# Kernel optimization log

Hardware: AMD Instinct MI355X
Metric: run time of the kernel (lower is better)

The kernel has to match this reference:

```python
import jax, jax.numpy as jnp
import numpy as np

EMBED_DIM = 768
NUM_HEADS = 12


def setup_inputs() -> dict:
    key = jax.random.key(0)
    k_x, k_w1, k_b1, k_w2, k_b2 = jax.random.split(key, 5)
    B, S, D = 4, 2048, EMBED_DIM
    s1 = 1.0 / np.sqrt(D)
    return {
        "x": jax.random.normal(k_x, (B, S, D), dtype=jnp.float32),
        "W1": jax.random.uniform(k_w1, (D, 3 * D), jnp.float32, -s1, s1),  # proj1 weight (in,out)
        "b1": jax.random.uniform(k_b1, (3 * D,), jnp.float32, -s1, s1),
        "W2": jax.random.uniform(k_w2, (D, D), jnp.float32, -s1, s1),  # proj2 weight (in,out)
        "b2": jax.random.uniform(k_b2, (D,), jnp.float32, -s1, s1),
    }


def reference(x, W1, b1, W2, b2):
    B, S, D = x.shape
    H = NUM_HEADS
    h = D // H
    qkv = x @ W1 + b1                       # [B,S,3D]
    qkv = qkv.reshape(B, S, H, 3 * h).transpose(0, 2, 1, 3)  # [B,H,S,3h]
    # chunk order in the original: K, Q, V
    K = qkv[..., :h]
    Q = qkv[..., h:2 * h]
    V = qkv[..., 2 * h:]
    # NOTE: original code computes Q @ V^T (not Q @ K^T) -- reproduced faithfully
    scores = jnp.einsum("bhqd,bhkd->bhqk", Q, V) / jnp.sqrt(jnp.float32(h))
    att = jax.nn.softmax(scores, axis=-1)
    out = jnp.einsum("bhqk,bhkd->bhqd", att, V)  # [B,H,S,h]
    out = out.transpose(0, 2, 1, 3).reshape(B, S, D)
    return out @ W2 + b2
```

## Files before the change

kernel.cpp:

```cpp
#include <hip/hip_runtime.h>
#include <hip/hip_bf16.h>
#include <math.h>


#define SEQ   2048
#define DIM   768
#define NHEAD 12
#define HDIM  64
#define BATCH 4

#define QSCALE 0.1803368801111244f

typedef __attribute__((ext_vector_type(8))) short s16x8;
typedef __attribute__((ext_vector_type(4))) float f32x4;

#if __has_builtin(__builtin_amdgcn_exp2f)
#define EXP2F(x) __builtin_amdgcn_exp2f(x)
#else
#define EXP2F(x) exp2f(x)
#endif

__device__ __forceinline__ unsigned short f2bf(float f) {
    union { float f; unsigned int u; } v; v.f = f;
    unsigned int r = v.u + 0x7fffu + ((v.u >> 16) & 1u);
    return (unsigned short)(r >> 16);
}

__device__ __forceinline__ unsigned int cvt_pk_bf16(float a, float b) {
    unsigned int r;
    asm("v_cvt_pk_bf16_f32 %0, %1, %2" : "=v"(r) : "v"(a), "v"(b));
    return r;
}

__device__ __forceinline__ void gload_lds16(const void* g, void* l) {
    __builtin_amdgcn_global_load_lds(
        (const __attribute__((address_space(1))) unsigned int*)g,
        (__attribute__((address_space(3))) unsigned int*)l, 16, 0, 0);
}

__global__ __launch_bounds__(256) void cvt_all(
    const float* __restrict__ x, const float* __restrict__ W1,
    const float* __restrict__ W2, unsigned short* __restrict__ xb,
    unsigned short* __restrict__ W1bt, unsigned short* __restrict__ W2bt)
{
    __shared__ float T[32][33];
    const int id = blockIdx.x;

    if (id >= 1728) {
        const size_t i4 = ((size_t)(id - 1728) * 256 + threadIdx.x) * 4;
        float4 v = *(const float4*)&x[i4];
        ushort4 o;
        o.x = f2bf(v.x); o.y = f2bf(v.y); o.z = f2bf(v.z); o.w = f2bf(v.w);
        *(ushort4*)&xb[i4] = o;
        return;
    }

    const float* W;
    unsigned short* out;
    int n0, k0, src_ld, c0;
    if (id < 1152) {
        W = W1; out = W1bt; src_ld = 2304;
        n0 = (id % 48) * 32; k0 = (id / 48) * 32;
        c0 = (n0 >> 7) * 192 + 64 + (n0 & 127);
    } else {
        const int id2 = id - 1152;
        W = W2; out = W2bt; src_ld = DIM;
        n0 = (id2 % 24) * 32; k0 = (id2 / 24) * 32;
        c0 = n0;
    }
    const int tc = threadIdx.x & 31, tr = threadIdx.x >> 5;
    #pragma unroll
    for (int i = 0; i < 4; ++i)
        T[tr + i * 8][tc] = W[(size_t)(k0 + tr + i * 8) * src_ld + c0 + tc];
    __syncthreads();
    #pragma unroll
    for (int i = 0; i < 4; ++i)
        out[(size_t)(n0 + tr + i * 8) * DIM + k0 + tc] = f2bf(T[tc][tr + i * 8]);
}

__device__ __forceinline__ void gemm128_loop(
    const unsigned short* __restrict__ A, const unsigned short* __restrict__ B,
    unsigned short* As, unsigned short* Bs, int m0, int n0, f32x4 acc[4][4])
{
    const int tid  = threadIdx.x;
    const int wave = tid >> 6;
    const int lane = tid & 63;
    const int quad = lane >> 4;
    const int lcol = lane & 15;
    const int wm = wave >> 1, wn = wave & 1;

    const int sr = lane >> 2;
    const int sp = lane & 3;
    const int sc = sp ^ ((sr >> 1) & 3);

    const int aswz = ((quad ^ ((lcol >> 1) & 3)) << 4);

    for (int k0 = 0; k0 < DIM; k0 += 32) {
        #pragma unroll
        for (int s = 0; s < 2; ++s) {
            const int r0 = wave * 32 + s * 16;
            gload_lds16(&A[(size_t)(m0 + r0 + sr) * DIM + k0 + sc * 8],
                        (void*)&As[r0 * 32]);
            gload_lds16(&B[(size_t)(n0 + r0 + sr) * DIM + k0 + sc * 8],
                        (void*)&Bs[r0 * 32]);
        }
        __syncthreads();

        s16x8 af[4], bf[4];
        #pragma unroll
        for (int mt = 0; mt < 4; ++mt) {
            const int row = wm * 64 + mt * 16 + lcol;
            af[mt] = *(const s16x8*)((const char*)As + row * 64 + aswz);
        }
        #pragma unroll
        for (int nt = 0; nt < 4; ++nt) {
            const int row = wn * 64 + nt * 16 + lcol;
            bf[nt] = *(const s16x8*)((const char*)Bs + row * 64 + aswz);
        }
        #pragma unroll
        for (int mt = 0; mt < 4; ++mt)
            #pragma unroll
            for (int nt = 0; nt < 4; ++nt)
                acc[mt][nt] = __builtin_amdgcn_mfma_f32_16x16x32_bf16(
                    af[mt], bf[nt], acc[mt][nt], 0, 0, 0);
        __syncthreads();
    }
}

__global__ __launch_bounds__(256) void qkv_gemm_bf16(
    const unsigned short* __restrict__ xb, const unsigned short* __restrict__ W1bt,
    const float* __restrict__ b1, unsigned short* __restrict__ Qb,
    unsigned short* __restrict__ Vr, unsigned short* __restrict__ Vt)
{
    __shared__ unsigned short LDSBUF[8192];
    f32x4 acc[4][4] = {};
    const int m0 = blockIdx.y * 128, n0 = blockIdx.x * 128;
    gemm128_loop(xb, W1bt, LDSBUF, LDSBUF + 4096, m0, n0, acc);

    const int tid  = threadIdx.x;
    const int wave = tid >> 6, lane = tid & 63;
    const int quad = lane >> 4, lcol = lane & 15;
    const int wm = wave >> 1, wn = wave & 1;

    const int colblock = n0 + wn * 64;
    const int head = colblock >> 7;
    const int cc0  = colblock & 127;
    const int isQ  = (cc0 == 0);
    const float scale = isQ ? QSCALE : 1.0f;
    unsigned short* dst = isQ ? Qb : Vr;

    float bias[4];
    #pragma unroll
    for (int nt = 0; nt < 4; ++nt)
        bias[nt] = b1[head * 192 + 64 + cc0 + nt * 16 + lcol];

    unsigned short* Wst = LDSBUF + wave * 2048;

    #pragma unroll
    for (int half = 0; half < 2; ++half) {
        #pragma unroll
        for (int mh = 0; mh < 2; ++mh) {
            const int mt = half * 2 + mh;
            #pragma unroll
            for (int nt = 0; nt < 4; ++nt)
                #pragma unroll
                for (int r = 0; r < 4; ++r) {
                    const float v = (acc[mt][nt][r] + bias[nt]) * scale;
                    Wst[(mh * 16 + quad * 4 + r) * 64 + nt * 16 + lcol] = f2bf(v);
                }
        }
        __syncthreads();
        #pragma unroll
        for (int p = 0; p < 4; ++p) {
            const int lr = p * 8 + (lane >> 3);
            const int c8 = (lane & 7) * 8;
            s16x8 v = *(const s16x8*)&Wst[lr * 64 + c8];
            const int m  = m0 + wm * 64 + half * 32 + lr;
            const int bb = m >> 11;
            const int s  = m & 2047;
            const int bhh = bb * NHEAD + head;
            *(s16x8*)&dst[((size_t)bhh * SEQ + s) * HDIM + c8] = v;
        }
        __syncthreads();
    }

    if (!isQ) {
        #pragma unroll
        for (int nt = 0; nt < 4; ++nt) {
            const int d = nt * 16 + lcol;
            #pragma unroll
            for (int mt = 0; mt < 4; ++mt) {
                const int m0r = m0 + wm * 64 + mt * 16 + quad * 4;
                const int bb  = m0r >> 11;
                const int s0  = m0r & 2047;
                const int bhh = bb * NHEAD + head;
                ushort4 o;
                o.x = f2bf(acc[mt][nt][0] + bias[nt]);
                o.y = f2bf(acc[mt][nt][1] + bias[nt]);
                o.z = f2bf(acc[mt][nt][2] + bias[nt]);
                o.w = f2bf(acc[mt][nt][3] + bias[nt]);
                *(ushort4*)&Vt[((size_t)bhh * HDIM + d) * SEQ + s0] = o;
            }
        }
    }
}

__global__ __launch_bounds__(256) void attn_mfma(
    const unsigned short* __restrict__ Qb, const unsigned short* __restrict__ Vr,
    const unsigned short* __restrict__ Vt, unsigned short* __restrict__ Yb)
{
    __shared__ unsigned short VrS[64 * 64];
    __shared__ unsigned short VtS[64 * 64];
    __shared__ unsigned short Ps[4][32 * 72];

    const int bh = blockIdx.x;
    const int b  = bh / NHEAD;
    const int hh = bh % NHEAD;
    const int q0 = blockIdx.y * 128;

    const int tid  = threadIdx.x;
    const int wave = tid >> 6;
    const int lane = tid & 63;
    const int quad = lane >> 4;
    const int lcol = lane & 15;

    s16x8 qa[2][2];
    #pragma unroll
    for (int mt = 0; mt < 2; ++mt)
        #pragma unroll
        for (int kk = 0; kk < 2; ++kk)
            qa[mt][kk] = *(const s16x8*)&Qb[((size_t)bh * SEQ + q0 + wave * 32 + mt * 16 + lcol) * HDIM
                                            + kk * 32 + quad * 8];

    s16x8 ones;
    #pragma unroll
    for (int i = 0; i < 8; ++i) ones[i] = (short)0x3F80;

    f32x4 oacc[2][4] = {};
    f32x4 lsum[2] = {};

    const int srow = lane >> 3;
    const int schk = (lane & 7) ^ srow;

    for (int k0 = 0; k0 < SEQ; k0 += 64) {
        #pragma unroll
        for (int s = 0; s < 2; ++s) {
            const int r0 = wave * 16 + s * 8;
            gload_lds16(&Vr[((size_t)bh * SEQ + k0 + r0 + srow) * HDIM + schk * 8],
                        (void*)&VrS[r0 * 64]);
            gload_lds16(&Vt[((size_t)bh * HDIM + r0 + srow) * SEQ + k0 + schk * 8],
                        (void*)&VtS[r0 * 64]);
        }
        __syncthreads();

        f32x4 sT[4][2] = {};
        #pragma unroll
        for (int kk = 0; kk < 2; ++kk) {
            s16x8 af[4];
            #pragma unroll
            for (int kt = 0; kt < 4; ++kt) {
                const int r = kt * 16 + lcol;
                const int c = kk * 4 + quad;
                af[kt] = *(const s16x8*)((const char*)VrS + r * 128 + ((c ^ (r & 7)) << 4));
            }
            #pragma unroll
            for (int kt = 0; kt < 4; ++kt)
                #pragma unroll
                for (int mt = 0; mt < 2; ++mt)
                    sT[kt][mt] = __builtin_amdgcn_mfma_f32_16x16x32_bf16(
                        af[kt], qa[mt][kk], sT[kt][mt], 0, 0, 0);
        }

        #pragma unroll
        for (int kt = 0; kt < 4; ++kt)
            #pragma unroll
            for (int mt = 0; mt < 2; ++mt) {
                const float p0 = EXP2F(sT[kt][mt][0]);
                const float p1 = EXP2F(sT[kt][mt][1]);
                const float p2 = EXP2F(sT[kt][mt][2]);
                const float p3 = EXP2F(sT[kt][mt][3]);
                uint2 w;
                w.x = cvt_pk_bf16(p0, p1);
                w.y = cvt_pk_bf16(p2, p3);
                *(uint2*)&Ps[wave][(mt * 16 + lcol) * 72 + kt * 16 + quad * 4] = w;
            }

        #pragma unroll
        for (int kk = 0; kk < 2; ++kk) {
            s16x8 pa[2];
            #pragma unroll
            for (int mt = 0; mt < 2; ++mt)
                pa[mt] = *(const s16x8*)&Ps[wave][(mt * 16 + lcol) * 72 + kk * 32 + quad * 8];
            #pragma unroll
            for (int mt = 0; mt < 2; ++mt)
                lsum[mt] = __builtin_amdgcn_mfma_f32_16x16x32_bf16(
                    pa[mt], ones, lsum[mt], 0, 0, 0);
            #pragma unroll
            for (int dt = 0; dt < 4; ++dt) {
                const int r = dt * 16 + lcol;
                const int c = kk * 4 + quad;
                s16x8 vb = *(const s16x8*)((const char*)VtS + r * 128 + ((c ^ (r & 7)) << 4));
                #pragma unroll
                for (int mt = 0; mt < 2; ++mt)
                    oacc[mt][dt] = __builtin_amdgcn_mfma_f32_16x16x32_bf16(
                        pa[mt], vb, oacc[mt][dt], 0, 0, 0);
            }
        }
        __syncthreads();
    }

    #pragma unroll
    for (int mt = 0; mt < 2; ++mt)
        #pragma unroll
        for (int r = 0; r < 4; ++r) {
            const float invl = 1.0f / lsum[mt][r];
            const int qrow = q0 + wave * 32 + mt * 16 + quad * 4 + r;
            #pragma unroll
            for (int dt = 0; dt < 4; ++dt)
                Yb[((size_t)b * SEQ + qrow) * DIM + hh * HDIM + dt * 16 + lcol] =
                    f2bf(oacc[mt][dt][r] * invl);
        }
}

__global__ __launch_bounds__(256) void proj_gemm_bf16(
    const unsigned short* __restrict__ Yb, const unsigned short* __restrict__ W2bt,
    const float* __restrict__ b2, float* __restrict__ out)
{
    __shared__ unsigned short LDSBUF[8192];
    unsigned short* As = LDSBUF;
    unsigned short* Bs = LDSBUF + 2048;

    const int tid  = threadIdx.x;
    const int wave = tid >> 6;
    const int lane = tid & 63;
    const int quad = lane >> 4;
    const int lcol = lane & 15;
    const int wm = wave >> 1, wn = wave & 1;

    const int m0 = blockIdx.y * 64, n0 = blockIdx.x * 128;

    const int sr = lane >> 2;
    const int sp = lane & 3;
    const int sc = sp ^ ((sr >> 1) & 3);
    const int aswz = ((quad ^ ((lcol >> 1) & 3)) << 4);

    f32x4 acc[2][4] = {};

    for (int k0 = 0; k0 < DIM; k0 += 32) {
        {
            const int r0 = wave * 16;
            gload_lds16(&Yb[(size_t)(m0 + r0 + sr) * DIM + k0 + sc * 8],
                        (void*)&As[r0 * 32]);
        }
        #pragma unroll
        for (int s = 0; s < 2; ++s) {
            const int r0 = wave * 32 + s * 16;
            gload_lds16(&W2bt[(size_t)(n0 + r0 + sr) * DIM + k0 + sc * 8],
                        (void*)&Bs[r0 * 32]);
        }
        __syncthreads();

        s16x8 af[2], bf[4];
        #pragma unroll
        for (int mt = 0; mt < 2; ++mt) {
            const int row = wm * 32 + mt * 16 + lcol;
            af[mt] = *(const s16x8*)((const char*)As + row * 64 + aswz);
        }
        #pragma unroll
        for (int nt = 0; nt < 4; ++nt) {
            const int row = wn * 64 + nt * 16 + lcol;
            bf[nt] = *(const s16x8*)((const char*)Bs + row * 64 + aswz);
        }
        #pragma unroll
        for (int mt = 0; mt < 2; ++mt)
            #pragma unroll
            for (int nt = 0; nt < 4; ++nt)
                acc[mt][nt] = __builtin_amdgcn_mfma_f32_16x16x32_bf16(
                    af[mt], bf[nt], acc[mt][nt], 0, 0, 0);
        __syncthreads();
    }

    float bias[4];
    #pragma unroll
    for (int nt = 0; nt < 4; ++nt)
        bias[nt] = b2[n0 + wn * 64 + nt * 16 + lcol];

    float* W32 = (float*)LDSBUF + wave * 1024;

    #pragma unroll
    for (int mt = 0; mt < 2; ++mt) {
        #pragma unroll
        for (int nt = 0; nt < 4; ++nt)
            #pragma unroll
            for (int r = 0; r < 4; ++r)
                W32[(quad * 4 + r) * 64 + nt * 16 + lcol] = acc[mt][nt][r] + bias[nt];
        __syncthreads();
        #pragma unroll
        for (int p = 0; p < 4; ++p) {
            const int lr = p * 4 + (lane >> 4);
            float4 v = *(const float4*)&W32[lr * 64 + (lane & 15) * 4];
            const int m = m0 + wm * 32 + mt * 16 + lr;
            *(float4*)&out[(size_t)m * DIM + n0 + wn * 64 + (lane & 15) * 4] = v;
        }
        __syncthreads();
    }
}

extern "C" void kernel_launch(void* const* d_in, const int* in_sizes, int n_in,
                              void* d_out, int out_size, void* d_ws, size_t ws_size,
                              hipStream_t stream)
{
    const float* x  = (const float*)d_in[0];
    const float* W1 = (const float*)d_in[1];
    const float* b1 = (const float*)d_in[2];
    const float* W2 = (const float*)d_in[3];
    const float* b2 = (const float*)d_in[4];
    float* out = (float*)d_out;

    const size_t NQV = (size_t)BATCH * NHEAD * SEQ * HDIM;
    unsigned short* Qb   = (unsigned short*)d_ws;
    unsigned short* Vr   = Qb + NQV;
    unsigned short* Vt   = Vr + NQV;
    unsigned short* Yb   = Vt + NQV;
    unsigned short* xb   = Yb + NQV;
    unsigned short* W1bt = xb + NQV;
    unsigned short* W2bt = W1bt + 1536 * DIM;

    cvt_all<<<7872, 256, 0, stream>>>(x, W1, W2, xb, W1bt, W2bt);

    qkv_gemm_bf16<<<dim3(12, 64), 256, 0, stream>>>(xb, W1bt, b1, Qb, Vr, Vt);
    attn_mfma<<<dim3(BATCH * NHEAD, SEQ / 128), 256, 0, stream>>>(Qb, Vr, Vt, Yb);
    proj_gemm_bf16<<<dim3(DIM / 128, 128), 256, 0, stream>>>(Yb, W2bt, b2, out);
}
```

Baseline: 214.9 us.

## Use two waves per attention block with 64 query rows each and swizzled P tile

```diff
diff --git a/kernel.cpp b/kernel.cpp
--- a/kernel.cpp
+++ b/kernel.cpp
@@ -205,13 +205,13 @@
     }
 }
 
-__global__ __launch_bounds__(256) void attn_mfma(
+__global__ __launch_bounds__(128) void attn_mfma(
     const unsigned short* __restrict__ Qb, const unsigned short* __restrict__ Vr,
     const unsigned short* __restrict__ Vt, unsigned short* __restrict__ Yb)
 {
     __shared__ unsigned short VrS[64 * 64];
     __shared__ unsigned short VtS[64 * 64];
-    __shared__ unsigned short Ps[4][32 * 72];
+    __shared__ unsigned short Ps[2][64 * 64];
 
     const int bh = blockIdx.x;
     const int b  = bh / NHEAD;
@@ -224,28 +224,31 @@
     const int quad = lane >> 4;
     const int lcol = lane & 15;
 
-    s16x8 qa[2][2];
-    #pragma unroll
-    for (int mt = 0; mt < 2; ++mt)
+    s16x8 qa[4][2];
+    #pragma unroll
+    for (int mt = 0; mt < 4; ++mt)
         #pragma unroll
         for (int kk = 0; kk < 2; ++kk)
-            qa[mt][kk] = *(const s16x8*)&Qb[((size_t)bh * SEQ + q0 + wave * 32 + mt * 16 + lcol) * HDIM
+            qa[mt][kk] = *(const s16x8*)&Qb[((size_t)bh * SEQ + q0 + wave * 64 + mt * 16 + lcol) * HDIM
                                             + kk * 32 + quad * 8];
 
     s16x8 ones;
     #pragma unroll
     for (int i = 0; i < 8; ++i) ones[i] = (short)0x3F80;
 
-    f32x4 oacc[2][4] = {};
-    f32x4 lsum[2] = {};
+    f32x4 oacc[4][4] = {};
+    f32x4 lsum[4] = {};
 
     const int srow = lane >> 3;
     const int schk = (lane & 7) ^ srow;
 
+    char* const Pw = (char*)&Ps[wave][0];
+    const int l7 = lcol & 7;
+
     for (int k0 = 0; k0 < SEQ; k0 += 64) {
         #pragma unroll
-        for (int s = 0; s < 2; ++s) {
-            const int r0 = wave * 16 + s * 8;
+        for (int s = 0; s < 4; ++s) {
+            const int r0 = wave * 32 + s * 8;
             gload_lds16(&Vr[((size_t)bh * SEQ + k0 + r0 + srow) * HDIM + schk * 8],
                         (void*)&VrS[r0 * 64]);
             gload_lds16(&Vt[((size_t)bh * HDIM + r0 + srow) * SEQ + k0 + schk * 8],
@@ -253,55 +256,59 @@
         }
         __syncthreads();
 
-        f32x4 sT[4][2] = {};
-        #pragma unroll
-        for (int kk = 0; kk < 2; ++kk) {
-            s16x8 af[4];
-            #pragma unroll
-            for (int kt = 0; kt < 4; ++kt) {
-                const int r = kt * 16 + lcol;
-                const int c = kk * 4 + quad;
-                af[kt] = *(const s16x8*)((const char*)VrS + r * 128 + ((c ^ (r & 7)) << 4));
+        #pragma unroll
+        for (int half = 0; half < 2; ++half) {
+            f32x4 sT[2][4] = {};
+            #pragma unroll
+            for (int kk = 0; kk < 2; ++kk) {
+                s16x8 af[2];
+                #pragma unroll
+                for (int t = 0; t < 2; ++t) {
+                    const int r = (half * 2 + t) * 16 + lcol;
+                    const int c = kk * 4 + quad;
+                    af[t] = *(const s16x8*)((const char*)VrS + r * 128 + ((c ^ (r & 7)) << 4));
+                }
+                #pragma unroll
+                for (int t = 0; t < 2; ++t)
+                    #pragma unroll
+                    for (int mt = 0; mt < 4; ++mt)
+                        sT[t][mt] = __builtin_amdgcn_mfma_f32_16x16x32_bf16(
+                            af[t], qa[mt][kk], sT[t][mt], 0, 0, 0);
             }
-            #pragma unroll
-            for (int kt = 0; kt < 4; ++kt)
+
+            #pragma unroll
+            for (int t = 0; t < 2; ++t) {
+                const int kt = half * 2 + t;
+                const int slot = (kt * 2 + (quad >> 1)) ^ l7;
                 #pragma unroll
-                for (int mt = 0; mt < 2; ++mt)
-                    sT[kt][mt] = __builtin_amdgcn_mfma_f32_16x16x32_bf16(
-                        af[kt], qa[mt][kk], sT[kt][mt], 0, 0, 0);
-        }
-
-        #pragma unroll
-        for (int kt = 0; kt < 4; ++kt)
-            #pragma unroll
-            for (int mt = 0; mt < 2; ++mt) {
-                const float p0 = EXP2F(sT[kt][mt][0]);
-                const float p1 = EXP2F(sT[kt][mt][1]);
-                const float p2 = EXP2F(sT[kt][mt][2]);
-                const float p3 = EXP2F(sT[kt][mt][3]);
-                uint2 w;
-                w.x = cvt_pk_bf16(p0, p1);
-                w.y = cvt_pk_bf16(p2, p3);
-                *(uint2*)&Ps[wave][(mt * 16 + lcol) * 72 + kt * 16 + quad * 4] = w;
+                for (int mt = 0; mt < 4; ++mt) {
+                    const float p0 = EXP2F(sT[t][mt][0]);
+                    const float p1 = EXP2F(sT[t][mt][1]);
+                    const float p2 = EXP2F(sT[t][mt][2]);
+                    const float p3 = EXP2F(sT[t][mt][3]);
+                    uint2 w;
+                    w.x = cvt_pk_bf16(p0, p1);
+                    w.y = cvt_pk_bf16(p2, p3);
+                    *(uint2*)(Pw + (mt * 16 + lcol) * 128 + slot * 16 + (quad & 1) * 8) = w;
+                }
             }
 
-        #pragma unroll
-        for (int kk = 0; kk < 2; ++kk) {
-            s16x8 pa[2];
-            #pragma unroll
-            for (int mt = 0; mt < 2; ++mt)
-                pa[mt] = *(const s16x8*)&Ps[wave][(mt * 16 + lcol) * 72 + kk * 32 + quad * 8];
-            #pragma unroll
-            for (int mt = 0; mt < 2; ++mt)
+            s16x8 pa[4];
+            #pragma unroll
+            for (int mt = 0; mt < 4; ++mt)
+                pa[mt] = *(const s16x8*)(Pw + (mt * 16 + lcol) * 128
+                                            + (((half * 4 + quad) ^ l7) << 4));
+            #pragma unroll
+            for (int mt = 0; mt < 4; ++mt)
                 lsum[mt] = __builtin_amdgcn_mfma_f32_16x16x32_bf16(
                     pa[mt], ones, lsum[mt], 0, 0, 0);
             #pragma unroll
             for (int dt = 0; dt < 4; ++dt) {
                 const int r = dt * 16 + lcol;
-                const int c = kk * 4 + quad;
+                const int c = half * 4 + quad;
                 s16x8 vb = *(const s16x8*)((const char*)VtS + r * 128 + ((c ^ (r & 7)) << 4));
                 #pragma unroll
-                for (int mt = 0; mt < 2; ++mt)
+                for (int mt = 0; mt < 4; ++mt)
                     oacc[mt][dt] = __builtin_amdgcn_mfma_f32_16x16x32_bf16(
                         pa[mt], vb, oacc[mt][dt], 0, 0, 0);
             }
@@ -310,11 +317,11 @@
     }
 
     #pragma unroll
-    for (int mt = 0; mt < 2; ++mt)
+    for (int mt = 0; mt < 4; ++mt)
         #pragma unroll
         for (int r = 0; r < 4; ++r) {
             const float invl = 1.0f / lsum[mt][r];
-            const int qrow = q0 + wave * 32 + mt * 16 + quad * 4 + r;
+            const int qrow = q0 + wave * 64 + mt * 16 + quad * 4 + r;
             #pragma unroll
             for (int dt = 0; dt < 4; ++dt)
                 Yb[((size_t)b * SEQ + qrow) * DIM + hh * HDIM + dt * 16 + lcol] =
@@ -429,6 +436,6 @@
     cvt_all<<<7872, 256, 0, stream>>>(x, W1, W2, xb, W1bt, W2bt);
 
     qkv_gemm_bf16<<<dim3(12, 64), 256, 0, stream>>>(xb, W1bt, b1, Qb, Vr, Vt);
-    attn_mfma<<<dim3(BATCH * NHEAD, SEQ / 128), 256, 0, stream>>>(Qb, Vr, Vt, Yb);
+    attn_mfma<<<dim3(BATCH * NHEAD, SEQ / 128), 128, 0, stream>>>(Qb, Vr, Vt, Yb);
     proj_gemm_bf16<<<dim3(DIM / 128, 128), 256, 0, stream>>>(Yb, W2bt, b2, out);
 }
```

Result: slower. 233.1 us (+8.5%).

## Double-buffer V tiles in attention with register prefetch of the next block

Applied to the files above, without the earlier changes.

```diff
diff --git a/kernel.cpp b/kernel.cpp
--- a/kernel.cpp
+++ b/kernel.cpp
@@ -209,8 +209,8 @@
     const unsigned short* __restrict__ Qb, const unsigned short* __restrict__ Vr,
     const unsigned short* __restrict__ Vt, unsigned short* __restrict__ Yb)
 {
-    __shared__ unsigned short VrS[64 * 64];
-    __shared__ unsigned short VtS[64 * 64];
+    __shared__ unsigned short VrS[2][64 * 64];
+    __shared__ unsigned short VtS[2][64 * 64];
     __shared__ unsigned short Ps[4][32 * 72];
 
     const int bh = blockIdx.x;
@@ -242,16 +242,36 @@
     const int srow = lane >> 3;
     const int schk = (lane & 7) ^ srow;
 
+    s16x8 rv[2], rt[2];
+    #pragma unroll
+    for (int s = 0; s < 2; ++s) {
+        const int r0 = wave * 16 + s * 8;
+        rv[s] = *(const s16x8*)&Vr[((size_t)bh * SEQ + r0 + srow) * HDIM + schk * 8];
+        rt[s] = *(const s16x8*)&Vt[((size_t)bh * HDIM + r0 + srow) * SEQ + schk * 8];
+    }
+    #pragma unroll
+    for (int s = 0; s < 2; ++s) {
+        const int r0 = wave * 16 + s * 8;
+        *(s16x8*)((char*)&VrS[0][r0 * 64] + lane * 16) = rv[s];
+        *(s16x8*)((char*)&VtS[0][r0 * 64] + lane * 16) = rt[s];
+    }
+    __syncthreads();
+
+    int cur = 0;
     for (int k0 = 0; k0 < SEQ; k0 += 64) {
-        #pragma unroll
-        for (int s = 0; s < 2; ++s) {
-            const int r0 = wave * 16 + s * 8;
-            gload_lds16(&Vr[((size_t)bh * SEQ + k0 + r0 + srow) * HDIM + schk * 8],
-                        (void*)&VrS[r0 * 64]);
-            gload_lds16(&Vt[((size_t)bh * HDIM + r0 + srow) * SEQ + k0 + schk * 8],
-                        (void*)&VtS[r0 * 64]);
-        }
-        __syncthreads();
+        const bool more = (k0 + 64 < SEQ);
+        if (more) {
+            #pragma unroll
+            for (int s = 0; s < 2; ++s) {
+                const int r0 = wave * 16 + s * 8;
+                rv[s] = *(const s16x8*)&Vr[((size_t)bh * SEQ + k0 + 64 + r0 + srow) * HDIM + schk * 8];
+                rt[s] = *(const s16x8*)&Vt[((size_t)bh * HDIM + r0 + srow) * SEQ + k0 + 64 + schk * 8];
+            }
+            __builtin_amdgcn_sched_barrier(0);
+        }
+
+        const unsigned short* VrC = &VrS[cur][0];
+        const unsigned short* VtC = &VtS[cur][0];
 
         f32x4 sT[4][2] = {};
         #pragma unroll
@@ -261,7 +281,7 @@
             for (int kt = 0; kt < 4; ++kt) {
                 const int r = kt * 16 + lcol;
                 const int c = kk * 4 + quad;
-                af[kt] = *(const s16x8*)((const char*)VrS + r * 128 + ((c ^ (r & 7)) << 4));
+                af[kt] = *(const s16x8*)((const char*)VrC + r * 128 + ((c ^ (r & 7)) << 4));
             }
             #pragma unroll
             for (int kt = 0; kt < 4; ++kt)
@@ -299,14 +319,25 @@
             for (int dt = 0; dt < 4; ++dt) {
                 const int r = dt * 16 + lcol;
                 const int c = kk * 4 + quad;
-                s16x8 vb = *(const s16x8*)((const char*)VtS + r * 128 + ((c ^ (r & 7)) << 4));
+                s16x8 vb = *(const s16x8*)((const char*)VtC + r * 128 + ((c ^ (r & 7)) << 4));
                 #pragma unroll
                 for (int mt = 0; mt < 2; ++mt)
                     oacc[mt][dt] = __builtin_amdgcn_mfma_f32_16x16x32_bf16(
                         pa[mt], vb, oacc[mt][dt], 0, 0, 0);
             }
         }
-        __syncthreads();
+
+        if (more) {
+            const int nb = cur ^ 1;
+            #pragma unroll
+            for (int s = 0; s < 2; ++s) {
+                const int r0 = wave * 16 + s * 8;
+                *(s16x8*)((char*)&VrS[nb][r0 * 64] + lane * 16) = rv[s];
+                *(s16x8*)((char*)&VtS[nb][r0 * 64] + lane * 16) = rt[s];
+            }
+        }
+        __syncthreads();
+        cur ^= 1;
     }
 
     #pragma unroll
```

Result: no change. 210.9 us (-1.9%).
